# Optimization experiments

Measured on AMD Instinct MI355X. Metric: run time of the kernel, lower is better.

The kernel has to match this reference:

```python
import jax, jax.numpy as jnp
import numpy as np

NEG_SLOPE = 0.2  # PyG GATConv default negative_slope
EPS = 1e-16     # PyG softmax denominator epsilon


def gat_conv(x, src, dst, W, a_src, a_dst, bias):
    """PyG GATConv (concat=True, dropout off). x:[N,Fin], src/dst:[E]."""
    N = x.shape[0]
    H, C = a_src.shape
    h = (x @ W).reshape(N, H, C)                      # per-head projected features
    es = jnp.einsum('nhc,hc->nh', h, a_src)           # alpha_src per node/head
    ed = jnp.einsum('nhc,hc->nh', h, a_dst)           # alpha_dst per node/head
    e = jax.nn.leaky_relu(es[src] + ed[dst], NEG_SLOPE)   # [E,H] edge scores
    # segment softmax over destination nodes (every node has a self loop)
    m = jax.ops.segment_max(e, dst, num_segments=N)
    p = jnp.exp(e - m[dst])
    denom = jax.ops.segment_sum(p, dst, num_segments=N)
    alpha = p / (denom[dst] + EPS)                    # [E,H]
    out = jax.ops.segment_sum(h[src] * alpha[:, :, None], dst, num_segments=N)
    return out.reshape(N, H * C) + bias


def _single_graph(x, ei, W1, a_src1, a_dst1, b1, W2, a_src2, a_dst2, b2):
    N = x.shape[0]
    loop = jnp.arange(N, dtype=ei.dtype)              # add_self_loops=True
    src = jnp.concatenate([ei[0], loop])
    dst = jnp.concatenate([ei[1], loop])
    h = jax.nn.relu(gat_conv(x, src, dst, W1, a_src1, a_dst1, b1))
    # F.dropout with p=0.0 is identity
    return gat_conv(h, src, dst, W2, a_src2, a_dst2, b2)


def setup_inputs() -> dict:
    key = jax.random.key(0)
    ks = jax.random.split(key, 9)
    B, N, E, F_in, H, C = 2, 20000, 320000, 128, 8, 64

    def glorot(k, shape):
        fan_in, fan_out = shape[-2] if len(shape) > 1 else shape[-1], shape[-1]
        s = np.sqrt(6.0 / (fan_in + fan_out)).astype(np.float32)
        return jax.random.uniform(k, shape, jnp.float32, -s, s)

    return {
        'xs': jax.random.normal(ks[0], (B, N, F_in), jnp.float32),
        'edge_indexs': jax.random.randint(ks[1], (B, 2, E), 0, N, jnp.int32),
        'W1': glorot(ks[2], (F_in, H * C)),
        'a_src1': glorot(ks[3], (H, C)),
        'a_dst1': glorot(ks[4], (H, C)),
        'b1': jnp.zeros((H * C,), jnp.float32),
        'W2': glorot(ks[5], (H * C, C)),
        'a_src2': glorot(ks[6], (1, C)),
        'a_dst2': glorot(ks[7], (1, C)),
        'b2': jnp.zeros((C,), jnp.float32),
    }


def reference(xs, edge_indexs, W1, a_src1, a_dst1, b1, W2, a_src2, a_dst2, b2):
    f = lambda x, ei: _single_graph(x, ei, W1, a_src1, a_dst1, b1, W2, a_src2, a_dst2, b2)
    return jax.vmap(f)(xs, edge_indexs)               # [B, N, C]
```

## Files before the change

### kernel.cpp

```cpp
#include <hip/hip_runtime.h>
#include <hip/hip_bf16.h>
#include <cstdint>

#define NEG_SLOPE 0.2f
#define SOFTMAX_EPS 1e-16f
#define NN 20000
#define EE 320000
#define CAP 48

typedef __hip_bfloat16 bf16;
typedef unsigned short ushort;
typedef short s8v __attribute__((ext_vector_type(8)));
typedef float f4v __attribute__((ext_vector_type(4)));
typedef float f2v __attribute__((ext_vector_type(2)));

static __device__ __forceinline__ float lo16(unsigned u) { return __uint_as_float(u << 16); }
static __device__ __forceinline__ float hi16(unsigned u) { return __uint_as_float(u & 0xffff0000u); }
static __device__ __forceinline__ ushort f2bf(float v) {
    bf16 h = __float2bfloat16(v);
    return *(ushort*)&h;
}

__global__ void prep_kernel(const float* __restrict__ W1, const float* __restrict__ W2,
                            ushort* __restrict__ w1hi, ushort* __restrict__ w1lo,
                            ushort* __restrict__ w2hi, ushort* __restrict__ w2lo,
                            int* __restrict__ count) {
    int bid = blockIdx.x;
    int t = threadIdx.x;
    if (bid >= 48) {
        int idx = (bid - 48) * 256 + t;
        if (idx < 2 * NN) count[idx] = 0;
        return;
    }
    __shared__ float T[32][65];
    const float* src; ushort *dhi, *dlo; int K, C, c0, k0;
    if (bid < 32) { src = W1; dhi = w1hi; dlo = w1lo; K = 128; C = 512; c0 = (bid & 7) * 64; k0 = (bid >> 3) * 32; }
    else          { src = W2; dhi = w2hi; dlo = w2lo; K = 512; C = 64;  c0 = 0;              k0 = (bid - 32) * 32; }
    for (int i = 0; i < 8; ++i) {
        int flat = t + i * 256;
        int k = flat >> 6, c = flat & 63;
        T[k][c] = src[(size_t)(k0 + k) * C + c0 + c];
    }
    __syncthreads();
    int c = t >> 2, j0 = (t & 3) * 8;
    unsigned hp[4], lp[4];
#pragma unroll
    for (int p = 0; p < 4; ++p) {
        float v0 = T[j0 + p * 2][c], v1 = T[j0 + p * 2 + 1][c];
        ushort h0 = f2bf(v0), h1 = f2bf(v1);
        float l0 = v0 - __uint_as_float((unsigned)h0 << 16);
        float l1 = v1 - __uint_as_float((unsigned)h1 << 16);
        hp[p] = (unsigned)h0 | ((unsigned)h1 << 16);
        lp[p] = (unsigned)f2bf(l0) | ((unsigned)f2bf(l1) << 16);
    }
    size_t o = (size_t)(c0 + c) * K + k0 + j0;
    *(uint4*)&dhi[o] = make_uint4(hp[0], hp[1], hp[2], hp[3]);
    *(uint4*)&dlo[o] = make_uint4(lp[0], lp[1], lp[2], lp[3]);
}

#define G1S 40
#define GEMM1_BLOCKS 1252
__global__ __launch_bounds__(256) void gemm1_scatter(
        const float* __restrict__ xs, const ushort* __restrict__ w1hi,
        const ushort* __restrict__ w1lo, const float* __restrict__ a_src,
        const float* __restrict__ a_dst, bf16* __restrict__ h1,
        float* __restrict__ es, float* __restrict__ ed,
        const int* __restrict__ ei, int* __restrict__ count,
        ushort* __restrict__ esrc) {
    __shared__ ushort lds[25600];
    int t = threadIdx.x;
    int bid = blockIdx.x;

    if (bid >= GEMM1_BLOCKS) {
        int idx = bid - GEMM1_BLOCKS;
        int b = idx / 1250;
        int e = (idx % 1250) * 256 + t;
        const int* srcA = ei + (size_t)b * 2 * EE;
        int s = srcA[e], d = srcA[EE + e];
        if ((unsigned)d >= NN || (unsigned)s >= NN) return;
        int pos = atomicAdd(&count[b * NN + d], 1);
        if (pos < CAP)
            esrc[((size_t)b * NN + d) * CAP + pos] = (ushort)s;
        return;
    }

    ushort* Xhi = lds;
    ushort* Xlo = lds + 2560;
    ushort* Whi = lds + 5120;
    ushort* Wlo = lds + 15360;
    int w = t >> 6, lane = t & 63, quad = lane >> 4, l16 = lane & 15;
    int b = bid / 626;
    int rem = bid % 626;
    int nhalf = rem / 313;
    int row0 = (rem % 313) * 64, nbase = nhalf * 256;
    const float* x = xs + (size_t)b * NN * 128;
    bf16*  h1b = h1 + (size_t)b * NN * 512;
    float* esb = es + (size_t)b * NN * 8;
    float* edb = ed + (size_t)b * NN * 8;

    f4v acc[16];
#pragma unroll
    for (int i = 0; i < 16; ++i) acc[i] = (f4v)0.f;

    for (int kc = 0; kc < 4; ++kc) {
        __syncthreads();
        {
            int row = t >> 2, c0 = (t & 3) * 8;
            float v[8];
            if (row0 + row < NN) {
                float4 A = *(const float4*)&x[(size_t)(row0 + row) * 128 + kc * 32 + c0];
                float4 B = *(const float4*)&x[(size_t)(row0 + row) * 128 + kc * 32 + c0 + 4];
                v[0] = A.x; v[1] = A.y; v[2] = A.z; v[3] = A.w;
                v[4] = B.x; v[5] = B.y; v[6] = B.z; v[7] = B.w;
            } else {
#pragma unroll
                for (int i = 0; i < 8; ++i) v[i] = 0.f;
            }
            unsigned hp[4], lp[4];
#pragma unroll
            for (int p = 0; p < 4; ++p) {
                ushort h0 = f2bf(v[p * 2]), h1_ = f2bf(v[p * 2 + 1]);
                float l0 = v[p * 2] - __uint_as_float((unsigned)h0 << 16);
                float l1 = v[p * 2 + 1] - __uint_as_float((unsigned)h1_ << 16);
                hp[p] = (unsigned)h0 | ((unsigned)h1_ << 16);
                lp[p] = (unsigned)f2bf(l0) | ((unsigned)f2bf(l1) << 16);
            }
            *(uint4*)&Xhi[row * G1S + c0] = make_uint4(hp[0], hp[1], hp[2], hp[3]);
            *(uint4*)&Xlo[row * G1S + c0] = make_uint4(lp[0], lp[1], lp[2], lp[3]);
        }
        {
            const ushort* sh = w1hi + (size_t)(nbase + t) * 128 + kc * 32;
            const ushort* sl = w1lo + (size_t)(nbase + t) * 128 + kc * 32;
            uint4 h0 = *(const uint4*)(sh), h1_ = *(const uint4*)(sh + 8);
            uint4 h2 = *(const uint4*)(sh + 16), h3 = *(const uint4*)(sh + 24);
            uint4 l0 = *(const uint4*)(sl), l1 = *(const uint4*)(sl + 8);
            uint4 l2 = *(const uint4*)(sl + 16), l3 = *(const uint4*)(sl + 24);
            *(uint4*)&Whi[t * G1S]      = h0; *(uint4*)&Whi[t * G1S + 8]  = h1_;
            *(uint4*)&Whi[t * G1S + 16] = h2; *(uint4*)&Whi[t * G1S + 24] = h3;
            *(uint4*)&Wlo[t * G1S]      = l0; *(uint4*)&Wlo[t * G1S + 8]  = l1;
            *(uint4*)&Wlo[t * G1S + 16] = l2; *(uint4*)&Wlo[t * G1S + 24] = l3;
        }
        __syncthreads();
        int arow = (w * 16 + l16) * G1S + quad * 8;
        s8v ahi = *(const s8v*)&Xhi[arow];
        s8v alo = *(const s8v*)&Xlo[arow];
#pragma unroll
        for (int ct = 0; ct < 16; ++ct) {
            int baddr = (ct * 16 + l16) * G1S + quad * 8;
            s8v bhi = *(const s8v*)&Whi[baddr];
            s8v blo = *(const s8v*)&Wlo[baddr];
            acc[ct] = __builtin_amdgcn_mfma_f32_16x16x32_bf16(ahi, bhi, acc[ct], 0, 0, 0);
            acc[ct] = __builtin_amdgcn_mfma_f32_16x16x32_bf16(ahi, blo, acc[ct], 0, 0, 0);
            acc[ct] = __builtin_amdgcn_mfma_f32_16x16x32_bf16(alo, bhi, acc[ct], 0, 0, 0);
        }
    }

#pragma unroll
    for (int hh = 0; hh < 4; ++hh) {
        float s4[4] = {0.f, 0.f, 0.f, 0.f}, d4[4] = {0.f, 0.f, 0.f, 0.f};
#pragma unroll
        for (int ct4 = 0; ct4 < 4; ++ct4) {
            int ct = hh * 4 + ct4;
            int c = nbase + ct * 16 + l16;
            float as = a_src[c], ad = a_dst[c];
#pragma unroll
            for (int r = 0; r < 4; ++r) { s4[r] += acc[ct][r] * as; d4[r] += acc[ct][r] * ad; }
        }
#pragma unroll
        for (int o = 1; o < 16; o <<= 1) {
#pragma unroll
            for (int r = 0; r < 4; ++r) {
                s4[r] += __shfl_xor(s4[r], o);
                d4[r] += __shfl_xor(d4[r], o);
            }
        }
        if (l16 == 0) {
            int head = nhalf * 4 + hh;
#pragma unroll
            for (int r = 0; r < 4; ++r) {
                int gr = row0 + w * 16 + quad * 4 + r;
                if (gr < NN) { esb[gr * 8 + head] = s4[r]; edb[gr * 8 + head] = d4[r]; }
            }
        }
    }

    __syncthreads();
    ushort* rp = lds + w * 4224;
#pragma unroll
    for (int ct = 0; ct < 16; ++ct)
#pragma unroll
        for (int r = 0; r < 4; ++r)
            rp[(quad * 4 + r) * 264 + ct * 16 + l16] = f2bf(acc[ct][r]);
#pragma unroll
    for (int i = 0; i < 8; ++i) {
        int idx = i * 512 + lane * 8;
        int row = idx >> 8, col = idx & 255;
        uint4 vv = *(const uint4*)&rp[row * 264 + col];
        int gr = row0 + w * 16 + row;
        if (gr < NN) *(uint4*)&h1b[(size_t)gr * 512 + nbase + col] = vv;
    }
}

#define G2S 72
__global__ __launch_bounds__(256) void gemm2_mfma(
        const bf16* __restrict__ a, const ushort* __restrict__ w2hi,
        const ushort* __restrict__ w2lo, const float* __restrict__ a_src,
        const float* __restrict__ a_dst, bf16* __restrict__ h2,
        float* __restrict__ es, float* __restrict__ ed) {
    __shared__ ushort lds[13824];
    ushort* AS  = lds;
    ushort* Whi = lds + 4608;
    ushort* Wlo = lds + 9216;

    int t = threadIdx.x;
    int w = t >> 6, lane = t & 63, quad = lane >> 4, l16 = lane & 15;
    int b = blockIdx.y;
    int row0 = blockIdx.x * 64;
    const bf16* ab = a + (size_t)b * NN * 512;
    bf16*  h2b = h2 + (size_t)b * NN * 64;
    float* esb = es + (size_t)b * NN;
    float* edb = ed + (size_t)b * NN;

    f4v acc[4];
#pragma unroll
    for (int i = 0; i < 4; ++i) acc[i] = (f4v)0.f;

    for (int kc = 0; kc < 8; ++kc) {
        __syncthreads();
        {
            int row = t >> 2, k0 = (t & 3) * 16;
            uint4 q0, q1;
            if (row0 + row < NN) {
                q0 = *(const uint4*)(ab + (size_t)(row0 + row) * 512 + kc * 64 + k0);
                q1 = *(const uint4*)(ab + (size_t)(row0 + row) * 512 + kc * 64 + k0 + 8);
            } else { q0 = make_uint4(0, 0, 0, 0); q1 = q0; }
            *(uint4*)&AS[row * G2S + k0]     = q0;
            *(uint4*)&AS[row * G2S + k0 + 8] = q1;
            const ushort* sh = w2hi + (size_t)row * 512 + kc * 64 + k0;
            const ushort* sl = w2lo + (size_t)row * 512 + kc * 64 + k0;
            *(uint4*)&Whi[row * G2S + k0]     = *(const uint4*)(sh);
            *(uint4*)&Whi[row * G2S + k0 + 8] = *(const uint4*)(sh + 8);
            *(uint4*)&Wlo[row * G2S + k0]     = *(const uint4*)(sl);
            *(uint4*)&Wlo[row * G2S + k0 + 8] = *(const uint4*)(sl + 8);
        }
        __syncthreads();
#pragma unroll
        for (int ks = 0; ks < 2; ++ks) {
            s8v av = *(const s8v*)&AS[(w * 16 + l16) * G2S + ks * 32 + quad * 8];
#pragma unroll
            for (int ct = 0; ct < 4; ++ct) {
                int baddr = (ct * 16 + l16) * G2S + ks * 32 + quad * 8;
                s8v bhi = *(const s8v*)&Whi[baddr];
                s8v blo = *(const s8v*)&Wlo[baddr];
                acc[ct] = __builtin_amdgcn_mfma_f32_16x16x32_bf16(av, bhi, acc[ct], 0, 0, 0);
                acc[ct] = __builtin_amdgcn_mfma_f32_16x16x32_bf16(av, blo, acc[ct], 0, 0, 0);
            }
        }
    }

    {
        float s4[4] = {0.f, 0.f, 0.f, 0.f}, d4[4] = {0.f, 0.f, 0.f, 0.f};
#pragma unroll
        for (int ct = 0; ct < 4; ++ct) {
            int c = ct * 16 + l16;
            float as = a_src[c], ad = a_dst[c];
#pragma unroll
            for (int r = 0; r < 4; ++r) { s4[r] += acc[ct][r] * as; d4[r] += acc[ct][r] * ad; }
        }
#pragma unroll
        for (int o = 1; o < 16; o <<= 1) {
#pragma unroll
            for (int r = 0; r < 4; ++r) {
                s4[r] += __shfl_xor(s4[r], o);
                d4[r] += __shfl_xor(d4[r], o);
            }
        }
        if (l16 == 0) {
#pragma unroll
            for (int r = 0; r < 4; ++r) {
                int gr = row0 + w * 16 + quad * 4 + r;
                if (gr < NN) { esb[gr] = s4[r]; edb[gr] = d4[r]; }
            }
        }
    }

    __syncthreads();
    ushort* rp = lds + w * 1152;
#pragma unroll
    for (int ct = 0; ct < 4; ++ct)
#pragma unroll
        for (int r = 0; r < 4; ++r)
            rp[(quad * 4 + r) * G2S + ct * 16 + l16] = f2bf(acc[ct][r]);
#pragma unroll
    for (int i = 0; i < 2; ++i) {
        int idx = i * 512 + lane * 8;
        int row = idx >> 6, col = idx & 63;
        uint4 vv = *(const uint4*)&rp[row * G2S + col];
        int gr = row0 + w * 16 + row;
        if (gr < NN) *(uint4*)&h2b[(size_t)gr * 64 + col] = vv;
    }
}

__global__ __launch_bounds__(256) void aggregate1_kernel(
        const bf16* __restrict__ h1, const float* __restrict__ es,
        const float* __restrict__ ed, const int* __restrict__ count,
        const ushort* __restrict__ esrc, const float* __restrict__ b1,
        bf16* __restrict__ out1) {
    __shared__ float alds[4][2][2][32];
    __shared__ unsigned offs[4][2][32];

    int t = threadIdx.x;
    int wv = t >> 6, lane = t & 63;
    int bid = blockIdx.x;
    int combo = bid & 7;
    int b = combo >> 2;
    int qtr = combo & 3;
    int nA = (bid >> 3) * 8 + wv * 2;
    int nd = lane >> 5;
    int slot = lane & 31;
    int n_lane = nA + nd;

    const bf16*  h1b = h1 + (size_t)b * NN * 512;
    const float* esb = es + (size_t)b * NN * 8;
    const float* edb = ed + (size_t)b * NN * 8;
    bf16* out1b = out1 + (size_t)b * NN * 512;

    int deg_e_lane = count[b * NN + n_lane];
    deg_e_lane = max(0, min(deg_e_lane, CAP));
    int degAe = __shfl(deg_e_lane, 0);
    int degBe = __shfl(deg_e_lane, 32);

    if (degAe > 31 || degBe > 31) {
        unsigned cb64 = (unsigned)qtr * 256u + (unsigned)lane * 4u;
        for (int k = 0; k < 2; ++k) {
            int nn = nA + k;
            int de = count[b * NN + nn];
            de = max(0, min(de, CAP));
            int dg = de + 1;
            bool act2 = lane < dg;
            int sr = act2 ? ((lane < de) ? (int)esrc[((size_t)b * NN + nn) * CAP + lane] : nn) : 0;
            float2 edv2 = *(const float2*)&edb[nn * 8 + qtr * 2];
            float2 esv2 = *(const float2*)((const char*)esb + ((unsigned)sr << 5) + (unsigned)qtr * 8u);
            float e0 = esv2.x + edv2.x; e0 = (e0 >= 0.f) ? e0 : NEG_SLOPE * e0; e0 = act2 ? e0 : -1e30f;
            float e1 = esv2.y + edv2.y; e1 = (e1 >= 0.f) ? e1 : NEG_SLOPE * e1; e1 = act2 ? e1 : -1e30f;
            float m0 = e0, m1 = e1;
#pragma unroll
            for (int o = 32; o > 0; o >>= 1) {
                m0 = fmaxf(m0, __shfl_xor(m0, o));
                m1 = fmaxf(m1, __shfl_xor(m1, o));
            }
            float p0 = act2 ? __expf(e0 - m0) : 0.f;
            float p1 = act2 ? __expf(e1 - m1) : 0.f;
            float s0 = p0, s1 = p1;
#pragma unroll
            for (int o = 32; o > 0; o >>= 1) {
                s0 += __shfl_xor(s0, o);
                s1 += __shfl_xor(s1, o);
            }
            float a0 = p0 / (s0 + SOFTMAX_EPS);
            float a1 = p1 / (s1 + SOFTMAX_EPS);
            f2v acc = {0.f, 0.f};
            for (int j = 0; j < dg; ++j) {
                int sj = __shfl(sr, j);
                float aw0 = __shfl(a0, j);
                float aw1 = __shfl(a1, j);
                float aw = (lane >= 32) ? aw1 : aw0;
                unsigned u = *(const unsigned*)((const char*)h1b + ((unsigned)sj << 10) + cb64);
                f2v tv = {lo16(u), hi16(u)};
                f2v wp2 = {aw, aw};
                acc += tv * wp2;
            }
            float2 bv2 = *(const float2*)&b1[qtr * 128 + lane * 2];
            union { ushort us[2]; unsigned u1; } pk;
            pk.us[0] = f2bf(fmaxf(acc.x + bv2.x, 0.f));
            pk.us[1] = f2bf(fmaxf(acc.y + bv2.y, 0.f));
            *(unsigned*)(out1b + (size_t)nn * 512 + qtr * 128 + lane * 2) = pk.u1;
        }
        return;
    }

    int deg = deg_e_lane + 1;
    bool act = slot < deg;
    size_t beg = ((size_t)b * NN + n_lane) * CAP;
    int sreg = act ? ((slot < deg_e_lane) ? (int)esrc[beg + slot] : n_lane) : 0;
    float2 edv = *(const float2*)&edb[n_lane * 8 + qtr * 2];
    float2 esv = *(const float2*)((const char*)esb + ((unsigned)sreg << 5) + (unsigned)qtr * 8u);
    float e0 = esv.x + edv.x; e0 = (e0 >= 0.f) ? e0 : NEG_SLOPE * e0; e0 = act ? e0 : -1e30f;
    float e1 = esv.y + edv.y; e1 = (e1 >= 0.f) ? e1 : NEG_SLOPE * e1; e1 = act ? e1 : -1e30f;
    float m0 = e0, m1 = e1;
#pragma unroll
    for (int o = 16; o > 0; o >>= 1) {
        m0 = fmaxf(m0, __shfl_xor(m0, o));
        m1 = fmaxf(m1, __shfl_xor(m1, o));
    }
    float p0 = act ? __expf(e0 - m0) : 0.f;
    float p1 = act ? __expf(e1 - m1) : 0.f;
    float s0 = p0, s1 = p1;
#pragma unroll
    for (int o = 16; o > 0; o >>= 1) {
        s0 += __shfl_xor(s0, o);
        s1 += __shfl_xor(s1, o);
    }
    offs[wv][nd][slot] = act ? ((unsigned)sreg << 10) : 0u;
    alds[wv][nd][0][slot] = p0 / (s0 + SOFTMAX_EPS);
    alds[wv][nd][1][slot] = p1 / (s1 + SOFTMAX_EPS);

    int mh = slot >> 4;
    const unsigned* op = &offs[wv][nd][0];
    const float*    wp = &alds[wv][nd][mh][0];
    unsigned cb = (unsigned)qtr * 256u + (unsigned)slot * 8u;
    const bf16* hb = h1b;
    int mdeg = max(degAe, degBe) + 1;
    int trips = (mdeg + 3) >> 2;
    int trips2 = (trips + 1) & ~1;

    f2v acc0 = {0.f, 0.f}, acc1 = {0.f, 0.f};
    uint2 A0, A1, A2, A3, B0, B1, B2, B3;
    float4 wA, wB;

#define GLOAD(dst, voff) \
    asm volatile("global_load_dwordx2 %0, %1, %2" : "=&v"(dst) : "v"(voff), "s"(hb))

#define LOADBANK(U0, U1, U2, U3, W4, blk) do { \
        int s_ = (blk) << 2; \
        uint4 ov_ = *(const uint4*)&op[s_]; \
        W4 = *(const float4*)&wp[s_]; \
        unsigned va_ = ov_.x + cb, vb_ = ov_.y + cb; \
        unsigned vc_ = ov_.z + cb, vd_ = ov_.w + cb; \
        GLOAD(U0, va_); GLOAD(U1, vb_); GLOAD(U2, vc_); GLOAD(U3, vd_); \
    } while (0)

#define WAITSB(nlit) do { \
        asm volatile("s_waitcnt vmcnt(" #nlit ")" ::: "memory"); \
        __builtin_amdgcn_sched_barrier(0); \
    } while (0)

#define ROW(U, W) do { \
        f2v wp_ = {W, W}; \
        f2v t0_ = {lo16(U.x), hi16(U.x)}; acc0 += t0_ * wp_; \
        f2v t1_ = {lo16(U.y), hi16(U.y)}; acc1 += t1_ * wp_; \
    } while (0)

#define CONSUME(U0, U1, U2, U3, W4) do { \
        ROW(U0, W4.x); ROW(U1, W4.y); ROW(U2, W4.z); ROW(U3, W4.w); \
    } while (0)

    LOADBANK(A0, A1, A2, A3, wA, 0);
    LOADBANK(B0, B1, B2, B3, wB, 1);
    for (int it = 0; it + 2 < trips2; it += 2) {
        WAITSB(4);
        CONSUME(A0, A1, A2, A3, wA); LOADBANK(A0, A1, A2, A3, wA, it + 2);
        WAITSB(4);
        CONSUME(B0, B1, B2, B3, wB); LOADBANK(B0, B1, B2, B3, wB, it + 3);
    }
    WAITSB(4);
    CONSUME(A0, A1, A2, A3, wA);
    WAITSB(0);
    CONSUME(B0, B1, B2, B3, wB);

#undef GLOAD
#undef LOADBANK
#undef WAITSB
#undef ROW
#undef CONSUME

    float4 bv = *(const float4*)&b1[qtr * 128 + slot * 4];
    union { ushort us[4]; uint2 u2; } pack;
    pack.us[0] = f2bf(fmaxf(acc0.x + bv.x, 0.f));
    pack.us[1] = f2bf(fmaxf(acc0.y + bv.y, 0.f));
    pack.us[2] = f2bf(fmaxf(acc1.x + bv.z, 0.f));
    pack.us[3] = f2bf(fmaxf(acc1.y + bv.w, 0.f));
    *(uint2*)(out1b + (size_t)n_lane * 512 + qtr * 128 + slot * 4) = pack.u2;
}

__global__ void aggregate2_kernel(const bf16* __restrict__ h2, const float* __restrict__ es,
                                  const float* __restrict__ ed, const int* __restrict__ count,
                                  const ushort* __restrict__ esrc, const float* __restrict__ bias2,
                                  float* __restrict__ out) {
    __shared__ float wl[4][64];
    __shared__ int slidx[4][64];
    int t = threadIdx.x;
    int wv = t >> 6, lane = t & 63;
    int bid = blockIdx.x;
    int xcd = bid & 7;
    int q = bid >> 3;
    int b = xcd >> 2;
    int n = (xcd & 3) * 5000 + q * 4 + wv;

    const bf16*  h2b = h2 + (size_t)b * NN * 64;
    const float* esb = es + (size_t)b * NN;
    const float* edb = ed + (size_t)b * NN;
    float* outb = out + (size_t)b * NN * 64;

    int deg_e = count[b * NN + n];
    deg_e = max(0, min(deg_e, CAP));
    int deg = deg_e + 1;
    size_t beg = ((size_t)b * NN + n) * CAP;
    float edn = edb[n];

    bool act = lane < deg;
    int sreg = act ? ((lane < deg_e) ? (int)esrc[beg + lane] : n) : 0;
    float ev = act ? esb[sreg] + edn : -1e30f;
    ev = (ev >= 0.f) ? ev : NEG_SLOPE * ev;
    if (!act) ev = -1e30f;
    float m = ev;
#pragma unroll
    for (int o = 32; o > 0; o >>= 1) m = fmaxf(m, __shfl_xor(m, o));
    float p = act ? __expf(ev - m) : 0.f;
    float sum = p;
#pragma unroll
    for (int o = 32; o > 0; o >>= 1) sum += __shfl_xor(sum, o);
    slidx[wv][lane] = sreg;
    wl[wv][lane] = p / (sum + SOFTMAX_EPS);

    float acc[4] = {0.f, 0.f, 0.f, 0.f};
    int grp = lane >> 4, ch4 = (lane & 15) * 4;
    int j = grp;
    for (; j + 4 < deg; j += 8) {
        int sA = slidx[wv][j];     float wA = wl[wv][j];
        int sB = slidx[wv][j + 4]; float wB = wl[wv][j + 4];
        uint2 uA = *(const uint2*)(h2b + (size_t)sA * 64 + ch4);
        uint2 uB = *(const uint2*)(h2b + (size_t)sB * 64 + ch4);
        acc[0] += wA * lo16(uA.x); acc[1] += wA * hi16(uA.x);
        acc[2] += wA * lo16(uA.y); acc[3] += wA * hi16(uA.y);
        acc[0] += wB * lo16(uB.x); acc[1] += wB * hi16(uB.x);
        acc[2] += wB * lo16(uB.y); acc[3] += wB * hi16(uB.y);
    }
    for (; j < deg; j += 4) {
        int s = slidx[wv][j];
        float wt = wl[wv][j];
        uint2 u = *(const uint2*)(h2b + (size_t)s * 64 + ch4);
        acc[0] += wt * lo16(u.x); acc[1] += wt * hi16(u.x);
        acc[2] += wt * lo16(u.y); acc[3] += wt * hi16(u.y);
    }
#pragma unroll
    for (int i = 0; i < 4; ++i) {
        acc[i] += __shfl_xor(acc[i], 16);
        acc[i] += __shfl_xor(acc[i], 32);
    }
    if (lane < 16) {
        float4 o4;
        o4.x = acc[0] + bias2[ch4 + 0];
        o4.y = acc[1] + bias2[ch4 + 1];
        o4.z = acc[2] + bias2[ch4 + 2];
        o4.w = acc[3] + bias2[ch4 + 3];
        *(float4*)&outb[(size_t)n * 64 + ch4] = o4;
    }
}

extern "C" void kernel_launch(void* const* d_in, const int* in_sizes, int n_in,
                              void* d_out, int out_size, void* d_ws, size_t ws_size,
                              hipStream_t stream) {
    const float* xs     = (const float*)d_in[0];
    const int*   ei     = (const int*)d_in[1];
    const float* W1     = (const float*)d_in[2];
    const float* a_src1 = (const float*)d_in[3];
    const float* a_dst1 = (const float*)d_in[4];
    const float* b1     = (const float*)d_in[5];
    const float* W2     = (const float*)d_in[6];
    const float* a_src2 = (const float*)d_in[7];
    const float* a_dst2 = (const float*)d_in[8];
    const float* b2     = (const float*)d_in[9];
    float* out = (float*)d_out;

    const int B = 2;

    uintptr_t p = (uintptr_t)d_ws;
    auto alloc = [&](size_t bytes) {
        void* r = (void*)p;
        p += (bytes + 255) & ~(size_t)255;
        return r;
    };
    bf16* h1   = (bf16*)alloc((size_t)B * NN * 512 * 2);
    bf16* out1 = (bf16*)alloc((size_t)B * NN * 512 * 2);
    char* unionA = (char*)alloc((size_t)B * NN * 64 * 2);
    float*  es1   = (float*)unionA;
    float*  ed1   = (float*)(unionA + 1280000);
    ushort* wt1hi = (ushort*)(unionA + 2560000);
    ushort* wt1lo = (ushort*)(unionA + 2560000 + 131072);
    bf16*   h2    = (bf16*)unionA;
    ushort* wt2hi = (ushort*)alloc((size_t)64 * 512 * 2);
    ushort* wt2lo = (ushort*)alloc((size_t)64 * 512 * 2);
    float* es2    = (float*)alloc((size_t)B * NN * 4);
    float* ed2    = (float*)alloc((size_t)B * NN * 4);
    int*   count  = (int*)alloc((size_t)B * NN * 4);
    ushort* esrc  = (ushort*)alloc((size_t)B * NN * CAP * 2);

    const int initBlocks = (2 * NN + 255) / 256;
    prep_kernel<<<48 + initBlocks, 256, 0, stream>>>(W1, W2, wt1hi, wt1lo, wt2hi, wt2lo, count);
    gemm1_scatter<<<GEMM1_BLOCKS + 2500, 256, 0, stream>>>(xs, wt1hi, wt1lo, a_src1, a_dst1,
                                                           h1, es1, ed1, ei, count, esrc);
    aggregate1_kernel<<<20000, 256, 0, stream>>>(h1, es1, ed1, count, esrc, b1, out1);
    gemm2_mfma<<<dim3(313, B), 256, 0, stream>>>(out1, wt2hi, wt2lo, a_src2, a_dst2, h2, es2, ed2);
    aggregate2_kernel<<<10000, 256, 0, stream>>>(h2, es2, ed2, count, esrc, b2, out);
}
```

Before: 258.2 us.

## Pipeline batches across stages by co-launching next batch's GEMM with current aggregation

Splits each stage's work by batch element and fuses independent work from adjacent stages into single launches: GEMM1 for batch 1 runs alongside aggregation1 for batch 0, GEMM2 for batch 0 alongside aggregation1 for batch 1, and so on. The aim is to fill idle compute units during memory-bound aggregation with compute-bound GEMM blocks and to cut tail effects, at the cost of one extra launch. h2 now aliases h1 with a 512-column stride, which relies on h1 of a batch being dead before h2 of that batch is written. The agg1 base pointer is also made wave-uniform via readfirstlane for the scalar-operand load asm. Mixing kernels with different LDS and register needs in one launch may lower occupancy for the aggregation blocks.

```diff
diff --git a/kernel.cpp b/kernel.cpp
--- a/kernel.cpp
+++ b/kernel.cpp
@@ -59,38 +59,18 @@
 }
 
 #define G1S 40
-#define GEMM1_BLOCKS 1252
-__global__ __launch_bounds__(256) void gemm1_scatter(
+static __device__ void gemm1_body(int b, int rem,
         const float* __restrict__ xs, const ushort* __restrict__ w1hi,
         const ushort* __restrict__ w1lo, const float* __restrict__ a_src,
         const float* __restrict__ a_dst, bf16* __restrict__ h1,
-        float* __restrict__ es, float* __restrict__ ed,
-        const int* __restrict__ ei, int* __restrict__ count,
-        ushort* __restrict__ esrc) {
+        float* __restrict__ es, float* __restrict__ ed) {
     __shared__ ushort lds[25600];
     int t = threadIdx.x;
-    int bid = blockIdx.x;
-
-    if (bid >= GEMM1_BLOCKS) {
-        int idx = bid - GEMM1_BLOCKS;
-        int b = idx / 1250;
-        int e = (idx % 1250) * 256 + t;
-        const int* srcA = ei + (size_t)b * 2 * EE;
-        int s = srcA[e], d = srcA[EE + e];
-        if ((unsigned)d >= NN || (unsigned)s >= NN) return;
-        int pos = atomicAdd(&count[b * NN + d], 1);
-        if (pos < CAP)
-            esrc[((size_t)b * NN + d) * CAP + pos] = (ushort)s;
-        return;
-    }
-
     ushort* Xhi = lds;
     ushort* Xlo = lds + 2560;
     ushort* Whi = lds + 5120;
     ushort* Wlo = lds + 15360;
     int w = t >> 6, lane = t & 63, quad = lane >> 4, l16 = lane & 15;
-    int b = bid / 626;
-    int rem = bid % 626;
     int nhalf = rem / 313;
     int row0 = (rem % 313) * 64, nbase = nhalf * 256;
     const float* x = xs + (size_t)b * NN * 128;
@@ -201,23 +181,35 @@
     }
 }
 
+static __device__ void scatter_body(int idx, const int* __restrict__ ei,
+                                    int* __restrict__ count, ushort* __restrict__ esrc) {
+    int t = threadIdx.x;
+    int b = idx / 1250;
+    int e = (idx % 1250) * 256 + t;
+    const int* srcA = ei + (size_t)b * 2 * EE;
+    int s = srcA[e], d = srcA[EE + e];
+    if ((unsigned)d >= NN || (unsigned)s >= NN) return;
+    int pos = atomicAdd(&count[b * NN + d], 1);
+    if (pos < CAP)
+        esrc[((size_t)b * NN + d) * CAP + pos] = (ushort)s;
+}
+
 #define G2S 72
-__global__ __launch_bounds__(256) void gemm2_mfma(
+static __device__ void gemm2_body(int b, int bx,
         const bf16* __restrict__ a, const ushort* __restrict__ w2hi,
         const ushort* __restrict__ w2lo, const float* __restrict__ a_src,
         const float* __restrict__ a_dst, bf16* __restrict__ h2,
         float* __restrict__ es, float* __restrict__ ed) {
-    __shared__ ushort lds[13824];
-    ushort* AS  = lds;
-    ushort* Whi = lds + 4608;
-    ushort* Wlo = lds + 9216;
+    __shared__ ushort lds2[13824];
+    ushort* AS  = lds2;
+    ushort* Whi = lds2 + 4608;
+    ushort* Wlo = lds2 + 9216;
 
     int t = threadIdx.x;
     int w = t >> 6, lane = t & 63, quad = lane >> 4, l16 = lane & 15;
-    int b = blockIdx.y;
-    int row0 = blockIdx.x * 64;
+    int row0 = bx * 64;
     const bf16* ab = a + (size_t)b * NN * 512;
-    bf16*  h2b = h2 + (size_t)b * NN * 64;
+    bf16*  h2b = h2 + (size_t)b * NN * 512;
     float* esb = es + (size_t)b * NN;
     float* edb = ed + (size_t)b * NN;
 
@@ -285,7 +277,7 @@
     }
 
     __syncthreads();
-    ushort* rp = lds + w * 1152;
+    ushort* rp = lds2 + w * 1152;
 #pragma unroll
     for (int ct = 0; ct < 4; ++ct)
 #pragma unroll
@@ -301,7 +293,7 @@
     }
 }
 
-__global__ __launch_bounds__(256) void aggregate1_kernel(
+static __device__ void agg1_body(int b, int j,
         const bf16* __restrict__ h1, const float* __restrict__ es,
         const float* __restrict__ ed, const int* __restrict__ count,
         const ushort* __restrict__ esrc, const float* __restrict__ b1,
@@ -311,11 +303,9 @@
 
     int t = threadIdx.x;
     int wv = t >> 6, lane = t & 63;
-    int bid = blockIdx.x;
-    int combo = bid & 7;
-    int b = combo >> 2;
-    int qtr = combo & 3;
-    int nA = (bid >> 3) * 8 + wv * 2;
+    int qtr = (j & 7) >> 1;
+    int qidx = (j >> 3) * 2 + (j & 1);
+    int nA = qidx * 8 + wv * 2;
     int nd = lane >> 5;
     int slot = lane & 31;
     int n_lane = nA + nd;
@@ -360,10 +350,10 @@
             float a0 = p0 / (s0 + SOFTMAX_EPS);
             float a1 = p1 / (s1 + SOFTMAX_EPS);
             f2v acc = {0.f, 0.f};
-            for (int j = 0; j < dg; ++j) {
-                int sj = __shfl(sr, j);
-                float aw0 = __shfl(a0, j);
-                float aw1 = __shfl(a1, j);
+            for (int jj = 0; jj < dg; ++jj) {
+                int sj = __shfl(sr, jj);
+                float aw0 = __shfl(a0, jj);
+                float aw1 = __shfl(a1, jj);
                 float aw = (lane >= 32) ? aw1 : aw0;
                 unsigned u = *(const unsigned*)((const char*)h1b + ((unsigned)sj << 10) + cb64);
                 f2v tv = {lo16(u), hi16(u)};
@@ -409,7 +399,10 @@
     const unsigned* op = &offs[wv][nd][0];
     const float*    wp = &alds[wv][nd][mh][0];
     unsigned cb = (unsigned)qtr * 256u + (unsigned)slot * 8u;
-    const bf16* hb = h1b;
+    uint64_t hbu = (uint64_t)(uintptr_t)h1b;
+    unsigned hb_lo = __builtin_amdgcn_readfirstlane((unsigned)hbu);
+    unsigned hb_hi = __builtin_amdgcn_readfirstlane((unsigned)(hbu >> 32));
+    uint64_t hbs = ((uint64_t)hb_hi << 32) | (uint64_t)hb_lo;
     int mdeg = max(degAe, degBe) + 1;
     int trips = (mdeg + 3) >> 2;
     int trips2 = (trips + 1) & ~1;
@@ -419,7 +412,7 @@
     float4 wA, wB;
 
 #define GLOAD(dst, voff) \
-    asm volatile("global_load_dwordx2 %0, %1, %2" : "=&v"(dst) : "v"(voff), "s"(hb))
+    asm volatile("global_load_dwordx2 %0, %1, %2" : "=&v"(dst) : "v"(voff), "s"(hbs))
 
 #define LOADBANK(U0, U1, U2, U3, W4, blk) do { \
         int s_ = (blk) << 2; \
@@ -473,21 +466,18 @@
     *(uint2*)(out1b + (size_t)n_lane * 512 + qtr * 128 + slot * 4) = pack.u2;
 }
 
-__global__ void aggregate2_kernel(const bf16* __restrict__ h2, const float* __restrict__ es,
-                                  const float* __restrict__ ed, const int* __restrict__ count,
-                                  const ushort* __restrict__ esrc, const float* __restrict__ bias2,
-                                  float* __restrict__ out) {
+static __device__ void agg2_body(int b, int j,
+        const bf16* __restrict__ h2, const float* __restrict__ es,
+        const float* __restrict__ ed, const int* __restrict__ count,
+        const ushort* __restrict__ esrc, const float* __restrict__ bias2,
+        float* __restrict__ out) {
     __shared__ float wl[4][64];
     __shared__ int slidx[4][64];
     int t = threadIdx.x;
     int wv = t >> 6, lane = t & 63;
-    int bid = blockIdx.x;
-    int xcd = bid & 7;
-    int q = bid >> 3;
-    int b = xcd >> 2;
-    int n = (xcd & 3) * 5000 + q * 4 + wv;
-
-    const bf16*  h2b = h2 + (size_t)b * NN * 64;
+    int n = (j & 3) * 5000 + (j >> 2) * 4 + wv;
+
+    const bf16*  h2b = h2 + (size_t)b * NN * 512;
     const float* esb = es + (size_t)b * NN;
     const float* edb = ed + (size_t)b * NN;
     float* outb = out + (size_t)b * NN * 64;
@@ -515,10 +505,10 @@
 
     float acc[4] = {0.f, 0.f, 0.f, 0.f};
     int grp = lane >> 4, ch4 = (lane & 15) * 4;
-    int j = grp;
-    for (; j + 4 < deg; j += 8) {
-        int sA = slidx[wv][j];     float wA = wl[wv][j];
-        int sB = slidx[wv][j + 4]; float wB = wl[wv][j + 4];
+    int jj = grp;
+    for (; jj + 4 < deg; jj += 8) {
+        int sA = slidx[wv][jj];     float wA = wl[wv][jj];
+        int sB = slidx[wv][jj + 4]; float wB = wl[wv][jj + 4];
         uint2 uA = *(const uint2*)(h2b + (size_t)sA * 64 + ch4);
         uint2 uB = *(const uint2*)(h2b + (size_t)sB * 64 + ch4);
         acc[0] += wA * lo16(uA.x); acc[1] += wA * hi16(uA.x);
@@ -526,9 +516,9 @@
         acc[0] += wB * lo16(uB.x); acc[1] += wB * hi16(uB.x);
         acc[2] += wB * lo16(uB.y); acc[3] += wB * hi16(uB.y);
     }
-    for (; j < deg; j += 4) {
-        int s = slidx[wv][j];
-        float wt = wl[wv][j];
+    for (; jj < deg; jj += 4) {
+        int s = slidx[wv][jj];
+        float wt = wl[wv][jj];
         uint2 u = *(const uint2*)(h2b + (size_t)s * 64 + ch4);
         acc[0] += wt * lo16(u.x); acc[1] += wt * hi16(u.x);
         acc[2] += wt * lo16(u.y); acc[3] += wt * hi16(u.y);
@@ -546,6 +536,49 @@
         o4.w = acc[3] + bias2[ch4 + 3];
         *(float4*)&outb[(size_t)n * 64 + ch4] = o4;
     }
+}
+
+__global__ __launch_bounds__(256) void mixA_kernel(
+        const float* xs, const ushort* w1hi, const ushort* w1lo,
+        const float* a_src, const float* a_dst, bf16* h1, float* es, float* ed,
+        const int* ei, int* count, ushort* esrc) {
+    int bid = blockIdx.x;
+    if (bid < 626) gemm1_body(0, bid, xs, w1hi, w1lo, a_src, a_dst, h1, es, ed);
+    else           scatter_body(bid - 626, ei, count, esrc);
+}
+
+__global__ __launch_bounds__(256) void mixB_kernel(
+        const float* xs, const ushort* w1hi, const ushort* w1lo,
+        const float* a_src, const float* a_dst, bf16* h1, float* es, float* ed,
+        const int* count, const ushort* esrc, const float* b1, bf16* out1) {
+    int bid = blockIdx.x;
+    if (bid < 626) gemm1_body(1, bid, xs, w1hi, w1lo, a_src, a_dst, h1, es, ed);
+    else           agg1_body(0, bid - 626, h1, es, ed, count, esrc, b1, out1);
+}
+
+__global__ __launch_bounds__(256) void mixC_kernel(
+        const bf16* out1, const ushort* w2hi, const ushort* w2lo,
+        const float* a_src2, const float* a_dst2, bf16* h2, float* es2, float* ed2,
+        const bf16* h1, const float* es1, const float* ed1,
+        const int* count, const ushort* esrc, const float* b1, bf16* out1w) {
+    int bid = blockIdx.x;
+    if (bid < 313) gemm2_body(0, bid, out1, w2hi, w2lo, a_src2, a_dst2, h2, es2, ed2);
+    else           agg1_body(1, bid - 313, h1, es1, ed1, count, esrc, b1, out1w);
+}
+
+__global__ __launch_bounds__(256) void mixD_kernel(
+        const bf16* out1, const ushort* w2hi, const ushort* w2lo,
+        const float* a_src2, const float* a_dst2, bf16* h2, float* es2, float* ed2,
+        const int* count, const ushort* esrc, const float* b2, float* out) {
+    int bid = blockIdx.x;
+    if (bid < 313) gemm2_body(1, bid, out1, w2hi, w2lo, a_src2, a_dst2, h2, es2, ed2);
+    else           agg2_body(0, bid - 313, h2, es2, ed2, count, esrc, b2, out);
+}
+
+__global__ __launch_bounds__(256) void agg2b1_kernel(
+        const bf16* h2, const float* es2, const float* ed2,
+        const int* count, const ushort* esrc, const float* b2, float* out) {
+    agg2_body(1, blockIdx.x, h2, es2, ed2, count, esrc, b2, out);
 }
 
 extern "C" void kernel_launch(void* const* d_in, const int* in_sizes, int n_in,
@@ -578,7 +611,7 @@
     float*  ed1   = (float*)(unionA + 1280000);
     ushort* wt1hi = (ushort*)(unionA + 2560000);
     ushort* wt1lo = (ushort*)(unionA + 2560000 + 131072);
-    bf16*   h2    = (bf16*)unionA;
+    bf16*   h2    = h1;
     ushort* wt2hi = (ushort*)alloc((size_t)64 * 512 * 2);
     ushort* wt2lo = (ushort*)alloc((size_t)64 * 512 * 2);
     float* es2    = (float*)alloc((size_t)B * NN * 4);
@@ -588,9 +621,14 @@
 
     const int initBlocks = (2 * NN + 255) / 256;
     prep_kernel<<<48 + initBlocks, 256, 0, stream>>>(W1, W2, wt1hi, wt1lo, wt2hi, wt2lo, count);
-    gemm1_scatter<<<GEMM1_BLOCKS + 2500, 256, 0, stream>>>(xs, wt1hi, wt1lo, a_src1, a_dst1,
-                                                           h1, es1, ed1, ei, count, esrc);
-    aggregate1_kernel<<<20000, 256, 0, stream>>>(h1, es1, ed1, count, esrc, b1, out1);
-    gemm2_mfma<<<dim3(313, B), 256, 0, stream>>>(out1, wt2hi, wt2lo, a_src2, a_dst2, h2, es2, ed2);
-    aggregate2_kernel<<<10000, 256, 0, stream>>>(h2, es2, ed2, count, esrc, b2, out);
-}
+    mixA_kernel<<<626 + 2500, 256, 0, stream>>>(xs, wt1hi, wt1lo, a_src1, a_dst1,
+                                                h1, es1, ed1, ei, count, esrc);
+    mixB_kernel<<<626 + 10000, 256, 0, stream>>>(xs, wt1hi, wt1lo, a_src1, a_dst1,
+                                                 h1, es1, ed1, count, esrc, b1, out1);
+    mixC_kernel<<<313 + 10000, 256, 0, stream>>>(out1, wt2hi, wt2lo, a_src2, a_dst2,
+                                                 h2, es2, ed2,
+                                                 h1, es1, ed1, count, esrc, b1, out1);
+    mixD_kernel<<<313 + 5000, 256, 0, stream>>>(out1, wt2hi, wt2lo, a_src2, a_dst2,
+                                                h2, es2, ed2, count, esrc, b2, out);
+    agg2b1_kernel<<<5000, 256, 0, stream>>>(h2, es2, ed2, count, esrc, b2, out);
+}
```

Measured after the change: 407.9 us. 57.9% more time.
